# Performance work log

Measured on AMD Instinct MI355X. Metric: run time of the kernel, lower is better.

Reference implementation:

```python
import jax, jax.numpy as jnp
import numpy as np

C = 256
C8 = C // 8


def setup_inputs() -> dict:
    key = jax.random.key(0)
    ks = jax.random.split(key, 9)
    B, H, W = 4, 64, 64
    s = 1.0 / np.sqrt(C)
    return {
        "pre_feat": jax.random.normal(ks[0], (B, C, H, W), jnp.float32),
        "post_feat": jax.random.normal(ks[1], (B, C, H, W), jnp.float32),
        "Wq": jax.random.normal(ks[2], (C8, C), jnp.float32) * s,
        "bq": jnp.zeros((C8,), jnp.float32),
        "Wk": jax.random.normal(ks[3], (C8, C), jnp.float32) * s,
        "bk": jnp.zeros((C8,), jnp.float32),
        "Wv": jax.random.normal(ks[4], (C, C), jnp.float32) * s,
        "bv": jnp.zeros((C,), jnp.float32),
        "gamma": jnp.zeros((1,), jnp.float32),
    }


def reference(pre_feat, post_feat, Wq, bq, Wk, bk, Wv, bv, gamma):
    B, Cc, H, W = pre_feat.shape
    N = H * W
    pre = pre_feat.reshape(B, Cc, N)    # (B, C, N)
    post = post_feat.reshape(B, Cc, N)
    # 1x1 convs == per-pixel linear projections
    q = jnp.einsum('dc,bcn->bdn', Wq, post) + bq[None, :, None]  # (B, C8, N)
    k = jnp.einsum('dc,bcn->bdn', Wk, pre) + bk[None, :, None]   # (B, C8, N)
    v = jnp.einsum('dc,bcn->bdn', Wv, pre) + bv[None, :, None]   # (B, C, N)
    # energy[b,i,j] = <q[b,:,i], k[b,:,j]>  (unscaled)
    energy = jnp.einsum('bdi,bdj->bij', q, k)                    # (B, N, N)
    attention = jax.nn.softmax(energy, axis=-1)
    # out[b,c,i] = sum_j v[b,c,j] * attention[b,i,j]
    out = jnp.einsum('bcj,bij->bci', v, attention).reshape(B, Cc, H, W)
    return gamma[0] * out + post_feat
```

## Files before the change

kernel.cpp:

```cpp
#include <hip/hip_runtime.h>
#include <hip/hip_bf16.h>

#define Bn 4
#define Cn 256
#define Dn 32
#define Nn 4096

typedef __bf16 bf16x8 __attribute__((ext_vector_type(8)));
typedef float f32x4 __attribute__((ext_vector_type(4)));

__device__ __forceinline__ float bf2f(unsigned short u) {
  unsigned int v = ((unsigned int)u) << 16;
  return __builtin_bit_cast(float, v);
}
__device__ __forceinline__ unsigned short f2bf(float f) {
  unsigned int v = __builtin_bit_cast(unsigned int, f);
  v += 0x7FFFu + ((v >> 16) & 1u);
  return (unsigned short)(v >> 16);
}
__device__ __forceinline__ unsigned int pk2(float a, float b) {
  union { __hip_bfloat162 h; unsigned int u; } x;
  x.h = __float22bfloat162_rn(make_float2(a, b));
  return x.u;
}
__device__ __forceinline__ bf16x8 ldfrag(const unsigned short* p) {
  return __builtin_bit_cast(bf16x8, *(const uint4*)p);
}
__device__ __forceinline__ uint4 pack8(const float* p) {
  float4 a = *(const float4*)p;
  float4 b = *(const float4*)(p + 4);
  union { unsigned int u2[4]; uint4 u; } x;
  x.u2[0] = pk2(a.x, a.y); x.u2[1] = pk2(a.z, a.w);
  x.u2[2] = pk2(b.x, b.y); x.u2[3] = pk2(b.z, b.w);
  return x.u;
}
__device__ __forceinline__ void async16(unsigned short* lds, const unsigned short* g) {
  __builtin_amdgcn_global_load_lds(
      (const __attribute__((address_space(1))) unsigned int*)g,
      (__attribute__((address_space(3))) unsigned int*)lds, 16, 0, 0);
}

__global__ __launch_bounds__(256) void wconv(
    const float* __restrict__ Wq, const float* __restrict__ Wk,
    const float* __restrict__ Wv,
    unsigned short* __restrict__ WqBf, unsigned short* __restrict__ WkBf,
    unsigned short* __restrict__ WvBf)
{
  const size_t base = ((size_t)blockIdx.x * 256 + threadIdx.x) * 8;
  if (base < 8192) {
    *(uint4*)(WqBf + base) = pack8(Wq + base);
  } else if (base < 16384) {
    *(uint4*)(WkBf + base - 8192) = pack8(Wk + base - 8192);
  } else {
    *(uint4*)(WvBf + base - 16384) = pack8(Wv + base - 16384);
  }
}

__global__ __launch_bounds__(256) void qkprep(
    const float* __restrict__ pre, const float* __restrict__ post,
    const unsigned short* __restrict__ WqBf, const float* __restrict__ bq,
    const unsigned short* __restrict__ WkBf, const float* __restrict__ bk,
    const unsigned short* __restrict__ WvBf, const float* __restrict__ bv,
    unsigned short* __restrict__ Qt, unsigned short* __restrict__ Kt,
    unsigned short* __restrict__ VBf)
{
  __shared__ __align__(16) unsigned short sV[256 * 40];

  const int tid = threadIdx.x;
  const int lane = tid & 63, w = tid >> 6;
  const int quad = lane >> 4, n16 = lane & 15;
  const int b = blockIdx.x >> 7;
  const int i0 = (blockIdx.x & 127) << 5;
  const int isub = w & 1, dh = w >> 1;
  const int i = i0 + isub * 16 + n16;

  const f32x4 zz = {0.f, 0.f, 0.f, 0.f};
  f32x4 aq = zz, ak = zz;
  f32x4 accv[8];
#pragma unroll
  for (int ct = 0; ct < 8; ct++) accv[ct] = zz;

  const float* postB = post + (size_t)b * Cn * Nn + i;
  const float* preB  = pre  + (size_t)b * Cn * Nn + i;

#pragma unroll
  for (int kc = 0; kc < 8; kc++) {
    const int c0 = kc * 32 + quad * 8;
    const float* pp = postB + (size_t)c0 * Nn;
    const float* pr = preB + (size_t)c0 * Nn;
    union { unsigned int u2[4]; bf16x8 v; } bp, bq8;
#pragma unroll
    for (int e2 = 0; e2 < 4; e2++) {
      float p0 = pp[(size_t)(2 * e2) * Nn], p1 = pp[(size_t)(2 * e2 + 1) * Nn];
      float r0 = pr[(size_t)(2 * e2) * Nn], r1 = pr[(size_t)(2 * e2 + 1) * Nn];
      bp.u2[e2] = pk2(p0, p1);
      bq8.u2[e2] = pk2(r0, r1);
    }
    bf16x8 awq = ldfrag(WqBf + (size_t)(dh * 16 + n16) * Cn + kc * 32 + quad * 8);
    bf16x8 awk = ldfrag(WkBf + (size_t)(dh * 16 + n16) * Cn + kc * 32 + quad * 8);
    aq = __builtin_amdgcn_mfma_f32_16x16x32_bf16(awq, bp.v, aq, 0, 0, 0);
    ak = __builtin_amdgcn_mfma_f32_16x16x32_bf16(awk, bq8.v, ak, 0, 0, 0);
#pragma unroll
    for (int ct = 0; ct < 8; ct++) {
      bf16x8 aw = ldfrag(WvBf + (size_t)(dh * 128 + ct * 16 + n16) * Cn + kc * 32 + quad * 8);
      accv[ct] = __builtin_amdgcn_mfma_f32_16x16x32_bf16(aw, bq8.v, accv[ct], 0, 0, 0);
    }
  }

  const float LOG2E = 1.44269504f;
  union { unsigned short s[4]; uint2 u; } oq, ok;
#pragma unroll
  for (int r = 0; r < 4; r++) {
    int d = dh * 16 + quad * 4 + r;
    oq.s[r] = f2bf((aq[r] + bq[d]) * LOG2E);
    ok.s[r] = f2bf(ak[r] + bk[d]);
  }
  *(uint2*)(Qt + ((size_t)b * Nn + i) * Dn + dh * 16 + quad * 4) = oq.u;
  *(uint2*)(Kt + ((size_t)b * Nn + i) * Dn + dh * 16 + quad * 4) = ok.u;

#pragma unroll
  for (int ct = 0; ct < 8; ct++) {
#pragma unroll
    for (int r = 0; r < 4; r++) {
      const int c = dh * 128 + ct * 16 + quad * 4 + r;
      sV[c * 40 + isub * 16 + n16] = f2bf(accv[ct][r] + bv[c]);
    }
  }
  __syncthreads();
#pragma unroll
  for (int k = 0; k < 4; k++) {
    const int slot = tid + k * 256;
    const int c = slot >> 2, seg = slot & 3;
    *(uint4*)(VBf + ((size_t)b * Cn + c) * Nn + i0 + seg * 8) =
        *(const uint4*)(sV + c * 40 + seg * 8);
  }
}

__global__ __launch_bounds__(256, 4) void flash_attn(
    const unsigned short* __restrict__ Qt, const unsigned short* __restrict__ Kt,
    const unsigned short* __restrict__ VBf,
    unsigned short* __restrict__ Opart, float* __restrict__ Lpart)
{
  __shared__ __align__(16) unsigned short sX[256 * 64];
  __shared__ __align__(16) unsigned short Pl[64 * 64];

  const int tid = threadIdx.x;
  const int lane = tid & 63, w = tid >> 6;
  const int quad = lane >> 4, n16 = lane & 15;
  const int b = blockIdx.x >> 8;
  const int js = (blockIdx.x >> 6) & 3;
  const int it = blockIdx.x & 63;
  const int i0 = it * 64;
  const int jbase = js * 1024;

  const bf16x8 qf = ldfrag(Qt + ((size_t)b * Nn + i0 + w * 16 + n16) * Dn + quad * 8);

  const f32x4 zz = {0.f, 0.f, 0.f, 0.f};
  f32x4 acc[4][4];
#pragma unroll
  for (int sub = 0; sub < 4; sub++)
#pragma unroll
    for (int ct = 0; ct < 4; ct++) acc[sub][ct] = zz;
  float lrow = 0.f;

  const size_t laneoff = (size_t)(lane >> 3) * Nn + (size_t)(((lane & 7) ^ (lane >> 3)) << 3);
  const unsigned short* preB = VBf + (size_t)b * Cn * Nn + laneoff;
  const int xsw = n16 & 7;
  const int xoff0 = (quad ^ xsw) << 3;
  const int xoff1 = ((4 + quad) ^ xsw) << 3;
  const int psw = (n16 & 7) << 3;

  for (int t = 0; t < 16; ++t) {
    const int j0 = jbase + t * 64;
    __syncthreads();
#pragma unroll
    for (int k = 0; k < 8; k++) {
      const int rb = (k * 4 + w) * 8;
      async16(sX + rb * 64 + (lane << 3), preB + (size_t)rb * Nn + j0);
    }
    {
      f32x4 sc[4];
#pragma unroll
      for (int jt = 0; jt < 4; jt++) {
        bf16x8 akf = ldfrag(Kt + ((size_t)b * Nn + j0 + jt * 16 + n16) * Dn + quad * 8);
        sc[jt] = __builtin_amdgcn_mfma_f32_16x16x32_bf16(akf, qf, zz, 0, 0, 0);
      }
      float ps = 0.f;
#pragma unroll
      for (int jt = 0; jt < 4; jt++) {
        float p0 = exp2f(fminf(sc[jt][0], 101.f));
        float p1 = exp2f(fminf(sc[jt][1], 101.f));
        float p2 = exp2f(fminf(sc[jt][2], 101.f));
        float p3 = exp2f(fminf(sc[jt][3], 101.f));
        ps += (p0 + p1) + (p2 + p3);
        union { unsigned int u2[2]; uint2 u; } pk;
        pk.u2[0] = pk2(p0, p1);
        pk.u2[1] = pk2(p2, p3);
        *(uint2*)&Pl[(size_t)(w * 16 + n16) * 64 + ((jt * 16 + quad * 4) ^ psw)] = pk.u;
      }
      ps += __shfl_xor(ps, 16);
      ps += __shfl_xor(ps, 32);
      lrow += ps;
    }
    __syncthreads();

#pragma unroll
    for (int kc = 0; kc < 2; kc++) {
      const int xo = kc ? xoff1 : xoff0;
      bf16x8 pB[4];
#pragma unroll
      for (int sub = 0; sub < 4; sub++)
        pB[sub] = ldfrag(&Pl[(size_t)(sub * 16 + n16) * 64 + ((kc * 32 + quad * 8) ^ psw)]);
#pragma unroll
      for (int ct = 0; ct < 4; ct++) {
        const int crow = w * 64 + ct * 16 + n16;
        bf16x8 av = ldfrag(&sX[crow * 64 + xo]);
        acc[0][ct] = __builtin_amdgcn_mfma_f32_16x16x32_bf16(av, pB[0], acc[0][ct], 0, 0, 0);
        acc[1][ct] = __builtin_amdgcn_mfma_f32_16x16x32_bf16(av, pB[1], acc[1][ct], 0, 0, 0);
        acc[2][ct] = __builtin_amdgcn_mfma_f32_16x16x32_bf16(av, pB[2], acc[2][ct], 0, 0, 0);
        acc[3][ct] = __builtin_amdgcn_mfma_f32_16x16x32_bf16(av, pB[3], acc[3][ct], 0, 0, 0);
      }
    }
  }

  const size_t pbase = (size_t)(js * 4 + b) * Nn;
  if (quad == 0) Lpart[pbase + i0 + w * 16 + n16] = lrow;
#pragma unroll
  for (int sub = 0; sub < 4; sub++) {
    const int i = i0 + sub * 16 + n16;
#pragma unroll
    for (int ct = 0; ct < 4; ct++) {
      union { unsigned int u2[2]; uint2 u; } pk;
      pk.u2[0] = pk2(acc[sub][ct][0], acc[sub][ct][1]);
      pk.u2[1] = pk2(acc[sub][ct][2], acc[sub][ct][3]);
      *(uint2*)(Opart + (pbase + i) * 256 + w * 64 + ct * 16 + quad * 4) = pk.u;
    }
  }
}

__global__ __launch_bounds__(256) void combine(
    const unsigned short* __restrict__ Opart, const float* __restrict__ Lpart,
    const float* __restrict__ post, const float* __restrict__ gamma,
    float* __restrict__ out)
{
  __shared__ float sT[64 * 65];
  __shared__ float sL[64];

  const int tid = threadIdx.x;
  const int b = blockIdx.x >> 8;
  const int rest = blockIdx.x & 255;
  const int i0 = (rest >> 2) * 64;
  const int c0 = (rest & 3) * 64;

  if (tid < 64) {
    float l = 0.f;
#pragma unroll
    for (int js = 0; js < 4; js++) l += Lpart[(size_t)(js * 4 + b) * Nn + i0 + tid];
    sL[tid] = 1.f / l;
  }
  __syncthreads();

#pragma unroll
  for (int pass = 0; pass < 2; pass++) {
    const int il = (tid >> 3) + pass * 32;
    const int c8 = (tid & 7) << 3;
    float a[8] = {0.f, 0.f, 0.f, 0.f, 0.f, 0.f, 0.f, 0.f};
#pragma unroll
    for (int js = 0; js < 4; js++) {
      uint4 uu = *(const uint4*)(Opart + ((size_t)(js * 4 + b) * Nn + i0 + il) * 256 + c0 + c8);
      const unsigned short* us = (const unsigned short*)&uu;
#pragma unroll
      for (int e = 0; e < 8; e++) a[e] += bf2f(us[e]);
    }
    const float inv = sL[il];
#pragma unroll
    for (int e = 0; e < 8; e++) sT[(c8 + e) * 65 + il] = a[e] * inv;
  }
  __syncthreads();

  const float g = gamma[0];
#pragma unroll
  for (int itr = 0; itr < 4; itr++) {
    const int slot = tid + itr * 256;
    const int cr = slot >> 4, i4 = (slot & 15) << 2;
    const size_t addr = ((size_t)b * Cn + c0 + cr) * Nn + i0 + i4;
    float4 pp = *(const float4*)(post + addr);
    float4 ov;
    ov.x = g * sT[cr * 65 + i4 + 0] + pp.x;
    ov.y = g * sT[cr * 65 + i4 + 1] + pp.y;
    ov.z = g * sT[cr * 65 + i4 + 2] + pp.z;
    ov.w = g * sT[cr * 65 + i4 + 3] + pp.w;
    *(float4*)(out + addr) = ov;
  }
}

extern "C" void kernel_launch(void* const* d_in, const int* in_sizes, int n_in,
                              void* d_out, int out_size, void* d_ws, size_t ws_size,
                              hipStream_t stream) {
  const float* pre   = (const float*)d_in[0];
  const float* post  = (const float*)d_in[1];
  const float* Wq    = (const float*)d_in[2];
  const float* bq    = (const float*)d_in[3];
  const float* Wk    = (const float*)d_in[4];
  const float* bk    = (const float*)d_in[5];
  const float* Wv    = (const float*)d_in[6];
  const float* bv    = (const float*)d_in[7];
  const float* gamma = (const float*)d_in[8];
  float* out = (float*)d_out;

  unsigned short* ws = (unsigned short*)d_ws;
  unsigned short* Qt    = ws;
  unsigned short* Kt    = Qt + (size_t)Bn * Nn * Dn;
  unsigned short* VBf   = Kt + (size_t)Bn * Nn * Dn;
  unsigned short* WqBf  = VBf + (size_t)Bn * Cn * Nn;
  unsigned short* WkBf  = WqBf + Dn * Cn;
  unsigned short* WvBf  = WkBf + Dn * Cn;
  float* Lpart = (float*)(WvBf + Cn * Cn);
  unsigned short* Opart = (unsigned short*)(Lpart + 4 * Bn * Nn);

  wconv<<<40, 256, 0, stream>>>(Wq, Wk, Wv, WqBf, WkBf, WvBf);
  qkprep<<<512, 256, 0, stream>>>(pre, post, WqBf, bq, WkBf, bk, WvBf, bv,
                                  Qt, Kt, VBf);
  flash_attn<<<1024, 256, 0, stream>>>(Qt, Kt, VBf, Opart, Lpart);
  combine<<<1024, 256, 0, stream>>>(Opart, Lpart, post, gamma, out);
}
```

Measured before the change: 186.9 us.

## Double-buffer V tiles with 32-wide steps and software-pipelined score phase

Shrinks the key tile from 64 to 32 columns and double-buffers the V tile in shared memory, so the async copy of the next tile is issued before the PV MFMAs on the current one. The score/exp phase for the next tile is moved after the PV phase, with one raw s_barrier instead of a second __syncthreads, and K fragments are prefetched a step ahead. The goal is to hide global-load latency and cut barrier stalls per step. The cost is twice as many iterations, tighter hand-placed waitcnt and barrier ordering, and different LDS swizzles that have to stay conflict-free.

```diff
diff --git a/kernel.cpp b/kernel.cpp
--- a/kernel.cpp
+++ b/kernel.cpp
@@ -141,8 +141,8 @@
     const unsigned short* __restrict__ VBf,
     unsigned short* __restrict__ Opart, float* __restrict__ Lpart)
 {
-  __shared__ __align__(16) unsigned short sX[256 * 64];
-  __shared__ __align__(16) unsigned short Pl[64 * 64];
+  __shared__ __align__(16) unsigned short sX[2][256 * 32];
+  __shared__ __align__(16) unsigned short Pl[64 * 32];
 
   const int tid = threadIdx.x;
   const int lane = tid & 63, w = tid >> 6;
@@ -163,65 +163,84 @@
     for (int ct = 0; ct < 4; ct++) acc[sub][ct] = zz;
   float lrow = 0.f;
 
-  const size_t laneoff = (size_t)(lane >> 3) * Nn + (size_t)(((lane & 7) ^ (lane >> 3)) << 3);
-  const unsigned short* preB = VBf + (size_t)b * Cn * Nn + laneoff;
-  const int xsw = n16 & 7;
-  const int xoff0 = (quad ^ xsw) << 3;
-  const int xoff1 = ((4 + quad) ^ xsw) << 3;
-  const int psw = (n16 & 7) << 3;
-
-  for (int t = 0; t < 16; ++t) {
-    const int j0 = jbase + t * 64;
+  const int x3 = n16 & 3;
+  const int xrd = (quad ^ x3) << 3;
+  const int row32 = (w * 16 + n16) * 32;
+  const int plw0 = row32 + ((((quad >> 1) + 0) ^ x3) << 3) + ((quad & 1) << 2);
+  const int plw1 = row32 + ((((quad >> 1) + 2) ^ x3) << 3) + ((quad & 1) << 2);
+  const unsigned short* pK = Kt + ((size_t)b * Nn + n16) * Dn + quad * 8;
+  const unsigned short* vb = VBf + (size_t)b * Cn * Nn;
+  size_t dmaoff[4];
+#pragma unroll
+  for (int k = 0; k < 4; k++) {
+    const int row = (k * 4 + w) * 16 + (lane >> 2);
+    dmaoff[k] = (size_t)row * Nn + (size_t)(((lane & 3) ^ ((lane >> 2) & 3)) << 3);
+  }
+
+#define S_PHASE(A0, A1, JT0)                                                  \
+  {                                                                           \
+    f32x4 sc0 = __builtin_amdgcn_mfma_f32_16x16x32_bf16((A0), qf, zz, 0, 0, 0); \
+    f32x4 sc1 = __builtin_amdgcn_mfma_f32_16x16x32_bf16((A1), qf, zz, 0, 0, 0); \
+    float q0 = exp2f(fminf(sc0[0], 101.f)), q1 = exp2f(fminf(sc0[1], 101.f)); \
+    float q2 = exp2f(fminf(sc0[2], 101.f)), q3 = exp2f(fminf(sc0[3], 101.f)); \
+    float q4 = exp2f(fminf(sc1[0], 101.f)), q5 = exp2f(fminf(sc1[1], 101.f)); \
+    float q6 = exp2f(fminf(sc1[2], 101.f)), q7 = exp2f(fminf(sc1[3], 101.f)); \
+    union { unsigned int u2[2]; uint2 u; } pka, pkb;                          \
+    pka.u2[0] = pk2(q0, q1); pka.u2[1] = pk2(q2, q3);                         \
+    pkb.u2[0] = pk2(q4, q5); pkb.u2[1] = pk2(q6, q7);                         \
+    *(uint2*)&Pl[plw0] = pka.u;                                               \
+    *(uint2*)&Pl[plw1] = pkb.u;                                               \
+    float ps = (q0 + q1) + (q2 + q3) + (q4 + q5) + (q6 + q7);                 \
+    ps += __shfl_xor(ps, 16);                                                 \
+    ps += __shfl_xor(ps, 32);                                                 \
+    lrow += ps;                                                               \
+  }
+
+  bf16x8 akf0 = ldfrag(pK + (size_t)jbase * Dn);
+  bf16x8 akf1 = ldfrag(pK + (size_t)(jbase + 16) * Dn);
+  __builtin_amdgcn_sched_barrier(0);
+#pragma unroll
+  for (int k = 0; k < 4; k++)
+    async16(&sX[0][(k * 4 + w) * 512], vb + dmaoff[k] + jbase);
+  __builtin_amdgcn_sched_barrier(0);
+  S_PHASE(akf0, akf1, 0)
+
+  for (int t = 0; t < 32; ++t) {
+    const int cur = t & 1;
     __syncthreads();
-#pragma unroll
-    for (int k = 0; k < 8; k++) {
-      const int rb = (k * 4 + w) * 8;
-      async16(sX + rb * 64 + (lane << 3), preB + (size_t)rb * Nn + j0);
+    if (t < 31) {
+      const int j0n = jbase + (t + 1) * 32;
+      akf0 = ldfrag(pK + (size_t)j0n * Dn);
+      akf1 = ldfrag(pK + (size_t)(j0n + 16) * Dn);
+      __builtin_amdgcn_sched_barrier(0);
+#pragma unroll
+      for (int k = 0; k < 4; k++)
+        async16(&sX[cur ^ 1][(k * 4 + w) * 512], vb + dmaoff[k] + j0n);
+      __builtin_amdgcn_sched_barrier(0);
     }
     {
-      f32x4 sc[4];
-#pragma unroll
-      for (int jt = 0; jt < 4; jt++) {
-        bf16x8 akf = ldfrag(Kt + ((size_t)b * Nn + j0 + jt * 16 + n16) * Dn + quad * 8);
-        sc[jt] = __builtin_amdgcn_mfma_f32_16x16x32_bf16(akf, qf, zz, 0, 0, 0);
-      }
-      float ps = 0.f;
-#pragma unroll
-      for (int jt = 0; jt < 4; jt++) {
-        float p0 = exp2f(fminf(sc[jt][0], 101.f));
-        float p1 = exp2f(fminf(sc[jt][1], 101.f));
-        float p2 = exp2f(fminf(sc[jt][2], 101.f));
-        float p3 = exp2f(fminf(sc[jt][3], 101.f));
-        ps += (p0 + p1) + (p2 + p3);
-        union { unsigned int u2[2]; uint2 u; } pk;
-        pk.u2[0] = pk2(p0, p1);
-        pk.u2[1] = pk2(p2, p3);
-        *(uint2*)&Pl[(size_t)(w * 16 + n16) * 64 + ((jt * 16 + quad * 4) ^ psw)] = pk.u;
-      }
-      ps += __shfl_xor(ps, 16);
-      ps += __shfl_xor(ps, 32);
-      lrow += ps;
-    }
-    __syncthreads();
-
-#pragma unroll
-    for (int kc = 0; kc < 2; kc++) {
-      const int xo = kc ? xoff1 : xoff0;
+      const unsigned short* sXc = sX[cur];
       bf16x8 pB[4];
 #pragma unroll
       for (int sub = 0; sub < 4; sub++)
-        pB[sub] = ldfrag(&Pl[(size_t)(sub * 16 + n16) * 64 + ((kc * 32 + quad * 8) ^ psw)]);
+        pB[sub] = ldfrag(&Pl[(sub * 16 + n16) * 32 + xrd]);
 #pragma unroll
       for (int ct = 0; ct < 4; ct++) {
-        const int crow = w * 64 + ct * 16 + n16;
-        bf16x8 av = ldfrag(&sX[crow * 64 + xo]);
+        bf16x8 av = ldfrag(&sXc[(w * 64 + ct * 16 + n16) * 32 + xrd]);
         acc[0][ct] = __builtin_amdgcn_mfma_f32_16x16x32_bf16(av, pB[0], acc[0][ct], 0, 0, 0);
         acc[1][ct] = __builtin_amdgcn_mfma_f32_16x16x32_bf16(av, pB[1], acc[1][ct], 0, 0, 0);
         acc[2][ct] = __builtin_amdgcn_mfma_f32_16x16x32_bf16(av, pB[2], acc[2][ct], 0, 0, 0);
         acc[3][ct] = __builtin_amdgcn_mfma_f32_16x16x32_bf16(av, pB[3], acc[3][ct], 0, 0, 0);
       }
     }
-  }
+    if (t < 31) {
+      asm volatile("s_waitcnt lgkmcnt(0)" ::: "memory");
+      __builtin_amdgcn_s_barrier();
+      __builtin_amdgcn_sched_barrier(0);
+      S_PHASE(akf0, akf1, t + 1)
+    }
+  }
+#undef S_PHASE
 
   const size_t pbase = (size_t)(js * 4 + b) * Nn;
   if (quad == 0) Lpart[pbase + i0 + w * 16 + n16] = lrow;
```

New measurement: 186.8 us. No clear change (-0.1%).

## Split flash attention over channel halves with smaller j-tiles for higher occupancy

Applied to the files above, without the earlier changes.

The attention kernel now splits the 256 value channels into two halves across separate blocks, doubling the grid, and steps through keys in 32-wide tiles instead of 64. Shared memory per block and the accumulator register count both shrink, so launch bounds can target 8 blocks per CU instead of 4. In exchange, each channel-half block recomputes the QK scores and exponentials, which doubles that part of the work, and there are twice as many loop iterations and barriers.

```diff
diff --git a/kernel.cpp b/kernel.cpp
--- a/kernel.cpp
+++ b/kernel.cpp
@@ -136,104 +136,101 @@
   }
 }
 
-__global__ __launch_bounds__(256, 4) void flash_attn(
+__global__ __launch_bounds__(256, 8) void flash_attn(
     const unsigned short* __restrict__ Qt, const unsigned short* __restrict__ Kt,
     const unsigned short* __restrict__ VBf,
     unsigned short* __restrict__ Opart, float* __restrict__ Lpart)
 {
-  __shared__ __align__(16) unsigned short sX[256 * 64];
-  __shared__ __align__(16) unsigned short Pl[64 * 64];
+  __shared__ __align__(16) unsigned short sX[128 * 32];
+  __shared__ __align__(16) unsigned short Pl[64 * 32];
 
   const int tid = threadIdx.x;
   const int lane = tid & 63, w = tid >> 6;
   const int quad = lane >> 4, n16 = lane & 15;
-  const int b = blockIdx.x >> 8;
-  const int js = (blockIdx.x >> 6) & 3;
-  const int it = blockIdx.x & 63;
+  const int blk = blockIdx.x;
+  const int cs = blk & 1;
+  const int js = (blk >> 1) & 3;
+  const int it = (blk >> 3) & 63;
+  const int b  = blk >> 9;
   const int i0 = it * 64;
   const int jbase = js * 1024;
 
   const bf16x8 qf = ldfrag(Qt + ((size_t)b * Nn + i0 + w * 16 + n16) * Dn + quad * 8);
 
   const f32x4 zz = {0.f, 0.f, 0.f, 0.f};
-  f32x4 acc[4][4];
-#pragma unroll
-  for (int sub = 0; sub < 4; sub++)
-#pragma unroll
-    for (int ct = 0; ct < 4; ct++) acc[sub][ct] = zz;
+  f32x4 acc[4][2];
+#pragma unroll
+  for (int sub = 0; sub < 4; sub++) {
+    acc[sub][0] = zz;
+    acc[sub][1] = zz;
+  }
   float lrow = 0.f;
 
-  const size_t laneoff = (size_t)(lane >> 3) * Nn + (size_t)(((lane & 7) ^ (lane >> 3)) << 3);
-  const unsigned short* preB = VBf + (size_t)b * Cn * Nn + laneoff;
-  const int xsw = n16 & 7;
-  const int xoff0 = (quad ^ xsw) << 3;
-  const int xoff1 = ((4 + quad) ^ xsw) << 3;
-  const int psw = (n16 & 7) << 3;
-
-  for (int t = 0; t < 16; ++t) {
-    const int j0 = jbase + t * 64;
+  const int swz = n16 & 3;
+  const int xrd = (quad ^ swz) << 3;
+  const unsigned short* pK = Kt + ((size_t)b * Nn + n16) * Dn + quad * 8;
+  const unsigned short* vb = VBf + ((size_t)b * Cn + cs * 128) * Nn;
+  size_t dmaoff[2];
+#pragma unroll
+  for (int k = 0; k < 2; k++) {
+    const int rl = lane >> 2;
+    dmaoff[k] = (size_t)((w * 2 + k) * 16 + rl) * Nn
+              + (size_t)(((lane & 3) ^ (rl & 3)) << 3);
+  }
+  const int plrow = (w * 16 + n16) * 32;
+  const int plw0 = plrow + ((((quad >> 1) + 0) ^ swz) << 3) + ((quad & 1) << 2);
+  const int plw1 = plrow + ((((quad >> 1) + 2) ^ swz) << 3) + ((quad & 1) << 2);
+
+  for (int t = 0; t < 32; ++t) {
+    const int j0 = jbase + t * 32;
     __syncthreads();
-#pragma unroll
-    for (int k = 0; k < 8; k++) {
-      const int rb = (k * 4 + w) * 8;
-      async16(sX + rb * 64 + (lane << 3), preB + (size_t)rb * Nn + j0);
-    }
+    async16(&sX[(w * 2 + 0) * 512], vb + dmaoff[0] + j0);
+    async16(&sX[(w * 2 + 1) * 512], vb + dmaoff[1] + j0);
     {
-      f32x4 sc[4];
-#pragma unroll
-      for (int jt = 0; jt < 4; jt++) {
-        bf16x8 akf = ldfrag(Kt + ((size_t)b * Nn + j0 + jt * 16 + n16) * Dn + quad * 8);
-        sc[jt] = __builtin_amdgcn_mfma_f32_16x16x32_bf16(akf, qf, zz, 0, 0, 0);
-      }
-      float ps = 0.f;
-#pragma unroll
-      for (int jt = 0; jt < 4; jt++) {
-        float p0 = exp2f(fminf(sc[jt][0], 101.f));
-        float p1 = exp2f(fminf(sc[jt][1], 101.f));
-        float p2 = exp2f(fminf(sc[jt][2], 101.f));
-        float p3 = exp2f(fminf(sc[jt][3], 101.f));
-        ps += (p0 + p1) + (p2 + p3);
-        union { unsigned int u2[2]; uint2 u; } pk;
-        pk.u2[0] = pk2(p0, p1);
-        pk.u2[1] = pk2(p2, p3);
-        *(uint2*)&Pl[(size_t)(w * 16 + n16) * 64 + ((jt * 16 + quad * 4) ^ psw)] = pk.u;
-      }
+      bf16x8 ak0 = ldfrag(pK + (size_t)j0 * Dn);
+      bf16x8 ak1 = ldfrag(pK + (size_t)(j0 + 16) * Dn);
+      f32x4 sc0 = __builtin_amdgcn_mfma_f32_16x16x32_bf16(ak0, qf, zz, 0, 0, 0);
+      f32x4 sc1 = __builtin_amdgcn_mfma_f32_16x16x32_bf16(ak1, qf, zz, 0, 0, 0);
+      float q0 = exp2f(fminf(sc0[0], 101.f)), q1 = exp2f(fminf(sc0[1], 101.f));
+      float q2 = exp2f(fminf(sc0[2], 101.f)), q3 = exp2f(fminf(sc0[3], 101.f));
+      float q4 = exp2f(fminf(sc1[0], 101.f)), q5 = exp2f(fminf(sc1[1], 101.f));
+      float q6 = exp2f(fminf(sc1[2], 101.f)), q7 = exp2f(fminf(sc1[3], 101.f));
+      union { unsigned int u2[2]; uint2 u; } pka, pkb;
+      pka.u2[0] = pk2(q0, q1); pka.u2[1] = pk2(q2, q3);
+      pkb.u2[0] = pk2(q4, q5); pkb.u2[1] = pk2(q6, q7);
+      *(uint2*)&Pl[plw0] = pka.u;
+      *(uint2*)&Pl[plw1] = pkb.u;
+      float ps = (q0 + q1) + (q2 + q3) + (q4 + q5) + (q6 + q7);
       ps += __shfl_xor(ps, 16);
       ps += __shfl_xor(ps, 32);
       lrow += ps;
     }
     __syncthreads();
 
-#pragma unroll
-    for (int kc = 0; kc < 2; kc++) {
-      const int xo = kc ? xoff1 : xoff0;
-      bf16x8 pB[4];
-#pragma unroll
-      for (int sub = 0; sub < 4; sub++)
-        pB[sub] = ldfrag(&Pl[(size_t)(sub * 16 + n16) * 64 + ((kc * 32 + quad * 8) ^ psw)]);
-#pragma unroll
-      for (int ct = 0; ct < 4; ct++) {
-        const int crow = w * 64 + ct * 16 + n16;
-        bf16x8 av = ldfrag(&sX[crow * 64 + xo]);
-        acc[0][ct] = __builtin_amdgcn_mfma_f32_16x16x32_bf16(av, pB[0], acc[0][ct], 0, 0, 0);
-        acc[1][ct] = __builtin_amdgcn_mfma_f32_16x16x32_bf16(av, pB[1], acc[1][ct], 0, 0, 0);
-        acc[2][ct] = __builtin_amdgcn_mfma_f32_16x16x32_bf16(av, pB[2], acc[2][ct], 0, 0, 0);
-        acc[3][ct] = __builtin_amdgcn_mfma_f32_16x16x32_bf16(av, pB[3], acc[3][ct], 0, 0, 0);
+    {
+      bf16x8 av0 = ldfrag(&sX[(w * 32 + n16) * 32 + xrd]);
+      bf16x8 av1 = ldfrag(&sX[(w * 32 + 16 + n16) * 32 + xrd]);
+#pragma unroll
+      for (int sub = 0; sub < 4; sub++) {
+        bf16x8 pB = ldfrag(&Pl[(sub * 16 + n16) * 32 + xrd]);
+        acc[sub][0] = __builtin_amdgcn_mfma_f32_16x16x32_bf16(av0, pB, acc[sub][0], 0, 0, 0);
+        acc[sub][1] = __builtin_amdgcn_mfma_f32_16x16x32_bf16(av1, pB, acc[sub][1], 0, 0, 0);
       }
     }
   }
 
   const size_t pbase = (size_t)(js * 4 + b) * Nn;
-  if (quad == 0) Lpart[pbase + i0 + w * 16 + n16] = lrow;
+  if (cs == 0 && quad == 0) Lpart[pbase + i0 + w * 16 + n16] = lrow;
 #pragma unroll
   for (int sub = 0; sub < 4; sub++) {
     const int i = i0 + sub * 16 + n16;
 #pragma unroll
-    for (int ct = 0; ct < 4; ct++) {
+    for (int ct = 0; ct < 2; ct++) {
+      const int c = cs * 128 + w * 32 + ct * 16 + quad * 4;
       union { unsigned int u2[2]; uint2 u; } pk;
       pk.u2[0] = pk2(acc[sub][ct][0], acc[sub][ct][1]);
       pk.u2[1] = pk2(acc[sub][ct][2], acc[sub][ct][3]);
-      *(uint2*)(Opart + (pbase + i) * 256 + w * 64 + ct * 16 + quad * 4) = pk.u;
+      *(uint2*)(Opart + (pbase + i) * 256 + c) = pk.u;
     }
   }
 }
@@ -321,6 +318,6 @@
   wconv<<<40, 256, 0, stream>>>(Wq, Wk, Wv, WqBf, WkBf, WvBf);
   qkprep<<<512, 256, 0, stream>>>(pre, post, WqBf, bq, WkBf, bk, WvBf, bv,
                                   Qt, Kt, VBf);
-  flash_attn<<<1024, 256, 0, stream>>>(Qt, Kt, VBf, Opart, Lpart);
+  flash_attn<<<2048, 256, 0, stream>>>(Qt, Kt, VBf, Opart, Lpart);
   combine<<<1024, 256, 0, stream>>>(Opart, Lpart, post, gamma, out);
 }
```

Result: slower. 204.4 us (+9.3%).
